# Optimization experiments

Hardware: AMD Instinct MI355X
Metric: run time of the kernel (lower is better)

Reference implementation:

```python
import jax, jax.numpy as jnp
import numpy as np

PROCESSING_STEPS = 3


def setup_inputs() -> dict:
    key = jax.random.key(0)
    ks = jax.random.split(key, 6)
    N, D, G = 500000, 128, 4096
    x = jax.random.normal(ks[0], (N, D), dtype=jnp.float32)
    # torch LSTM param layout: [4*hidden, input] and [4*hidden, hidden], gates i,f,g,o
    s = 1.0 / np.sqrt(D)
    W_ih = jax.random.uniform(ks[1], (4 * D, 2 * D), minval=-s, maxval=s, dtype=jnp.float32)
    W_hh = jax.random.uniform(ks[2], (4 * D, D), minval=-s, maxval=s, dtype=jnp.float32)
    b_ih = jax.random.uniform(ks[3], (4 * D,), minval=-s, maxval=s, dtype=jnp.float32)
    b_hh = jax.random.uniform(ks[4], (4 * D,), minval=-s, maxval=s, dtype=jnp.float32)
    index = jnp.sort(jax.random.randint(ks[5], (N,), 0, G, dtype=jnp.int64))
    return {"x": x, "W_ih": W_ih, "W_hh": W_hh, "b_ih": b_ih, "b_hh": b_hh,
            "index": index, "dim_size": G}


def _lstm_cell(inp, h, c, W_ih, W_hh, b_ih, b_hh):
    gates = inp @ W_ih.T + h @ W_hh.T + (b_ih + b_hh)  # [G, 4D]
    i, f, g, o = jnp.split(gates, 4, axis=-1)
    c = jax.nn.sigmoid(f) * c + jax.nn.sigmoid(i) * jnp.tanh(g)
    h = jax.nn.sigmoid(o) * jnp.tanh(c)
    return h, c


def reference(x, W_ih, W_hh, b_ih, b_hh, index, dim_size):
    N, D = x.shape
    h = jnp.zeros((dim_size, D), dtype=x.dtype)
    c = jnp.zeros((dim_size, D), dtype=x.dtype)
    q_star = jnp.zeros((dim_size, 2 * D), dtype=x.dtype)
    for _ in range(PROCESSING_STEPS):
        h, c = _lstm_cell(q_star, h, c, W_ih, W_hh, b_ih, b_hh)
        q = h  # [G, D]
        e = jnp.sum(x * q[index], axis=-1)  # [N]
        # segment softmax (numerically stable)
        m = jax.ops.segment_max(e, index, num_segments=dim_size)
        m = jnp.where(jnp.isfinite(m), m, 0.0)  # guard empty segments
        ex = jnp.exp(e - m[index])
        s = jax.ops.segment_sum(ex, index, num_segments=dim_size)
        a = ex / jnp.maximum(s, 1e-16)[index]  # [N]
        r = jax.ops.segment_sum(a[:, None] * x, index, num_segments=dim_size)  # [G, D]
        q_star = jnp.concatenate([q, r], axis=-1)
    return q_star
```

## Files before the change

### kernel.cpp

```cpp
#include <hip/hip_runtime.h>
#include <math.h>

#define D 128

__device__ __forceinline__ float sigmoidf_(float x) { return 1.f / (1.f + __expf(-x)); }

__global__ void seg_bounds_kernel(const int* __restrict__ idx, int N, int G,
                                  int* __restrict__ seg_off) {
    int g = blockIdx.x * blockDim.x + threadIdx.x;
    if (g > G) return;
    int lo = 0, hi = N;
    while (lo < hi) {
        int mid = (lo + hi) >> 1;
        if (idx[mid] < g) lo = mid + 1; else hi = mid;
    }
    seg_off[g] = lo;
}

__global__ void prep_wc_kernel(const float* __restrict__ W_ih, const float* __restrict__ W_hh,
                               float* __restrict__ Wc) {
    int t = blockIdx.x * blockDim.x + threadIdx.x;
    if (t >= 4 * D * D) return;
    int j = t >> 7;
    int k = t & (D - 1);
    Wc[t] = W_ih[(size_t)j * (2 * D) + k] + W_hh[t];
}

__global__ void prep_bias_kernel(const float* __restrict__ b_ih, const float* __restrict__ b_hh,
                                 float* __restrict__ b_sum, float* __restrict__ h1,
                                 float* __restrict__ c1) {
    int t = threadIdx.x;
    float b = b_ih[t] + b_hh[t];
    b_sum[t] = b;
    if (t < D) {
        float bi = b_ih[t] + b_hh[t];
        float bg = b_ih[2 * D + t] + b_hh[2 * D + t];
        float bo = b_ih[3 * D + t] + b_hh[3 * D + t];
        float c = sigmoidf_(bi) * tanhf(bg);
        c1[t] = c;
        h1[t] = sigmoidf_(bo) * tanhf(c);
    }
}

__global__ void base2_kernel(const float* __restrict__ Wc, const float* __restrict__ b_sum,
                             const float* __restrict__ h1, float* __restrict__ base2) {
    __shared__ float hs[D];
    int j = blockIdx.x * 256 + threadIdx.x;
    if (threadIdx.x < D) hs[threadIdx.x] = h1[threadIdx.x];
    __syncthreads();
    float acc = 0.f;
    const float4* w4 = (const float4*)(Wc + (size_t)j * D);
#pragma unroll 8
    for (int k4 = 0; k4 < D / 4; ++k4) {
        float4 w = w4[k4];
        const float* hp = &hs[k4 * 4];
        acc += w.x * hp[0] + w.y * hp[1] + w.z * hp[2] + w.w * hp[3];
    }
    base2[j] = b_sum[j] + acc;
}

__global__ __launch_bounds__(64) void attn_kernel(
    const float* __restrict__ x,
    const int* __restrict__ seg_off,
    const float* __restrict__ q,
    int q_stride,
    float* __restrict__ r_out, int r_stride,
    int G) {
    int g = blockIdx.x;
    if (g >= G) return;
    int lane = threadIdx.x;
    const float2* x2 = (const float2*)x;
    const float2* q2 = (const float2*)(q + (size_t)g * q_stride);
    float2 qv = q2[lane];
    int start = seg_off[g], end = seg_off[g + 1];

    float m = -INFINITY, s = 0.f;
    float2 acc; acc.x = 0.f; acc.y = 0.f;

    int n = start;
    for (; n + 2 <= end; n += 2) {
        float2 x0 = x2[(size_t)n * 64 + lane];
        float2 x1 = x2[(size_t)(n + 1) * 64 + lane];
        float p0 = x0.x * qv.x + x0.y * qv.y;
        float p1 = x1.x * qv.x + x1.y * qv.y;
#pragma unroll
        for (int off = 1; off < 64; off <<= 1) {
            p0 += __shfl_xor(p0, off);
            p1 += __shfl_xor(p1, off);
        }
        float mn = fmaxf(m, fmaxf(p0, p1));
        float al = __expf(m - mn);
        float w0 = __expf(p0 - mn);
        float w1 = __expf(p1 - mn);
        s = s * al + w0 + w1;
        acc.x = acc.x * al + w0 * x0.x + w1 * x1.x;
        acc.y = acc.y * al + w0 * x0.y + w1 * x1.y;
        m = mn;
    }
    if (n < end) {
        float2 x0 = x2[(size_t)n * 64 + lane];
        float p0 = x0.x * qv.x + x0.y * qv.y;
#pragma unroll
        for (int off = 1; off < 64; off <<= 1) p0 += __shfl_xor(p0, off);
        float mn = fmaxf(m, p0);
        float al = __expf(m - mn);
        float w0 = __expf(p0 - mn);
        s = s * al + w0;
        acc.x = acc.x * al + w0 * x0.x;
        acc.y = acc.y * al + w0 * x0.y;
    }
    float inv = 1.f / fmaxf(s, 1e-16f);
    float2 r; r.x = acc.x * inv; r.y = acc.y * inv;
    *(float2*)&r_out[(size_t)g * r_stride + 2 * lane] = r;
}

__global__ __launch_bounds__(256) void gates_gemm_kernel(
    const float* __restrict__ A1,
    const float* __restrict__ W1,
    const float* __restrict__ A2,
    const float* __restrict__ W2,
    int sW2,
    const float* __restrict__ bias,
    float* __restrict__ gates) {
    __shared__ float As[16][132];
    __shared__ float Ws[16][132];
    int t = threadIdx.x;
    int tx = t & 15, ty = t >> 4;
    int g0 = blockIdx.x * 128, j0 = blockIdx.y * 128;
    int lr = t >> 1;
    int lk = (t & 1) * 8;

    float acc[8][8];
#pragma unroll
    for (int i = 0; i < 8; ++i)
#pragma unroll
        for (int j = 0; j < 8; ++j) acc[i][j] = 0.f;

    for (int phase = 0; phase < 2; ++phase) {
        const float* A = phase ? A2 : A1;
        if (A == nullptr) continue;
        const float* W = phase ? W2 : W1;
        int sW = phase ? sW2 : D;
        for (int kk = 0; kk < D; kk += 16) {
            float4 a0 = *(const float4*)&A[(size_t)(g0 + lr) * D + kk + lk];
            float4 a1 = *(const float4*)&A[(size_t)(g0 + lr) * D + kk + lk + 4];
            float4 w0 = *(const float4*)&W[(size_t)(j0 + lr) * sW + kk + lk];
            float4 w1 = *(const float4*)&W[(size_t)(j0 + lr) * sW + kk + lk + 4];
            __syncthreads();
            As[lk + 0][lr] = a0.x; As[lk + 1][lr] = a0.y; As[lk + 2][lr] = a0.z; As[lk + 3][lr] = a0.w;
            As[lk + 4][lr] = a1.x; As[lk + 5][lr] = a1.y; As[lk + 6][lr] = a1.z; As[lk + 7][lr] = a1.w;
            Ws[lk + 0][lr] = w0.x; Ws[lk + 1][lr] = w0.y; Ws[lk + 2][lr] = w0.z; Ws[lk + 3][lr] = w0.w;
            Ws[lk + 4][lr] = w1.x; Ws[lk + 5][lr] = w1.y; Ws[lk + 6][lr] = w1.z; Ws[lk + 7][lr] = w1.w;
            __syncthreads();
#pragma unroll
            for (int k = 0; k < 16; ++k) {
                float4 a0v = *(const float4*)&As[k][ty * 8];
                float4 a1v = *(const float4*)&As[k][ty * 8 + 4];
                float4 b0v = *(const float4*)&Ws[k][tx * 8];
                float4 b1v = *(const float4*)&Ws[k][tx * 8 + 4];
                float av[8] = {a0v.x, a0v.y, a0v.z, a0v.w, a1v.x, a1v.y, a1v.z, a1v.w};
                float bv[8] = {b0v.x, b0v.y, b0v.z, b0v.w, b1v.x, b1v.y, b1v.z, b1v.w};
#pragma unroll
                for (int i = 0; i < 8; ++i)
#pragma unroll
                    for (int j = 0; j < 8; ++j)
                        acc[i][j] = fmaf(av[i], bv[j], acc[i][j]);
            }
        }
    }
#pragma unroll
    for (int i = 0; i < 8; ++i) {
        size_t row = (size_t)(g0 + ty * 8 + i);
        float4 o0, o1;
        int jb = j0 + tx * 8;
        o0.x = acc[i][0] + bias[jb + 0]; o0.y = acc[i][1] + bias[jb + 1];
        o0.z = acc[i][2] + bias[jb + 2]; o0.w = acc[i][3] + bias[jb + 3];
        o1.x = acc[i][4] + bias[jb + 4]; o1.y = acc[i][5] + bias[jb + 5];
        o1.z = acc[i][6] + bias[jb + 6]; o1.w = acc[i][7] + bias[jb + 7];
        *(float4*)&gates[row * 512 + jb] = o0;
        *(float4*)&gates[row * 512 + jb + 4] = o1;
    }
}

__global__ void cell_kernel(const float* __restrict__ gates,
                            const float* __restrict__ c_prev, int c_stride,
                            float* __restrict__ c_out,
                            float* __restrict__ h_out, int h_stride,
                            int total) {
    int t = blockIdx.x * blockDim.x + threadIdx.x;
    if (t >= total) return;
    int g = t >> 7, k = t & (D - 1);
    const float* grow = gates + (size_t)g * 512;
    float ig = grow[k];
    float fg = grow[D + k];
    float gg = grow[2 * D + k];
    float og = grow[3 * D + k];
    float cp = c_prev[(size_t)g * c_stride + k];
    float c = sigmoidf_(fg) * cp + sigmoidf_(ig) * tanhf(gg);
    float h = sigmoidf_(og) * tanhf(c);
    c_out[t] = c;
    h_out[(size_t)g * h_stride + k] = h;
}

extern "C" void kernel_launch(void* const* d_in, const int* in_sizes, int n_in,
                              void* d_out, int out_size, void* d_ws, size_t ws_size,
                              hipStream_t stream) {
    const float* x      = (const float*)d_in[0];
    const float* W_ih   = (const float*)d_in[1];
    const float* W_hh   = (const float*)d_in[2];
    const float* b_ih   = (const float*)d_in[3];
    const float* b_hh   = (const float*)d_in[4];
    const int*   index  = (const int*)d_in[5];
    int N = in_sizes[5];
    int G = out_size / (2 * D);
    float* out = (float*)d_out;

    float* ws = (float*)d_ws;
    float* Wc     = ws;
    float* b_sum  = Wc + 4 * D * D;
    float* h1     = b_sum + 4 * D;
    float* c1     = h1 + D;
    float* base2  = c1 + D;
    float* r1     = base2 + 4 * D;
    float* h2     = r1 + (size_t)G * D;
    float* c2     = h2 + (size_t)G * D;
    float* r2     = c2 + (size_t)G * D;
    float* gatesb = r2 + (size_t)G * D;
    int* seg_off  = (int*)(gatesb + (size_t)G * 4 * D);
    float* c3     = r1;

    seg_bounds_kernel<<<(G + 1 + 255) / 256, 256, 0, stream>>>(index, N, G, seg_off);
    prep_wc_kernel<<<(4 * D * D + 255) / 256, 256, 0, stream>>>(W_ih, W_hh, Wc);
    prep_bias_kernel<<<1, 512, 0, stream>>>(b_ih, b_hh, b_sum, h1, c1);
    base2_kernel<<<2, 256, 0, stream>>>(Wc, b_sum, h1, base2);

    attn_kernel<<<G, 64, 0, stream>>>(x, seg_off, h1, 0, r1, D, G);

    gates_gemm_kernel<<<dim3(G / 128, 4), 256, 0, stream>>>(
        nullptr, Wc, r1, W_ih + D, 2 * D, base2, gatesb);
    cell_kernel<<<(G * D + 255) / 256, 256, 0, stream>>>(gatesb, c1, 0, c2, h2, D, G * D);
    attn_kernel<<<G, 64, 0, stream>>>(x, seg_off, h2, D, r2, D, G);

    gates_gemm_kernel<<<dim3(G / 128, 4), 256, 0, stream>>>(
        h2, Wc, r2, W_ih + D, 2 * D, b_sum, gatesb);
    cell_kernel<<<(G * D + 255) / 256, 256, 0, stream>>>(gatesb, c2, D, c3, out, 2 * D, G * D);
    attn_kernel<<<G, 64, 0, stream>>>(x, seg_off, out, 2 * D, out + D, 2 * D, G);
}
```

Measured before the change: 581.2 us.

## Split each segment's attention across four waves with float4 loads and prefetch

The attention kernel now uses 256 threads per segment instead of 64. Each of four wavefronts handles a contiguous quarter of the segment's rows, and the partial online-softmax states (max, sum, accumulator) are merged through shared memory. Within a wave, each half-wave processes one row with float4 loads, and the next pair of rows is prefetched in software. The aim is more memory-level parallelism on the bandwidth-bound x streaming, with a shorter shuffle reduction. In exchange it adds a block-level sync, shared-memory merge overhead, and more threads per small segment (about 122 rows per segment).

```diff
diff --git a/kernel.cpp b/kernel.cpp
--- a/kernel.cpp
+++ b/kernel.cpp
@@ -59,7 +59,7 @@
     base2[j] = b_sum[j] + acc;
 }
 
-__global__ __launch_bounds__(64) void attn_kernel(
+__global__ __launch_bounds__(256) void attn_kernel(
     const float* __restrict__ x,
     const int* __restrict__ seg_off,
     const float* __restrict__ q,
@@ -68,50 +68,82 @@
     int G) {
     int g = blockIdx.x;
     if (g >= G) return;
-    int lane = threadIdx.x;
-    const float2* x2 = (const float2*)x;
-    const float2* q2 = (const float2*)(q + (size_t)g * q_stride);
-    float2 qv = q2[lane];
+    int tid = threadIdx.x;
+    int wave = tid >> 6, lane = tid & 63;
+    int half = lane >> 5;
+    int col4 = lane & 31;
+
+    __shared__ float sm[4], ss[4];
+    __shared__ float sacc[4][D];
+
     int start = seg_off[g], end = seg_off[g + 1];
+    int count = end - start;
+    int chunk = (count + 3) >> 2;
+    int wsr = start + wave * chunk;
+    int wer = min(wsr + chunk, end);
+
+    const float4* x4 = (const float4*)x;
+    const float4* q4 = (const float4*)(q + (size_t)g * q_stride);
+    float4 qv = q4[col4];
 
     float m = -INFINITY, s = 0.f;
-    float2 acc; acc.x = 0.f; acc.y = 0.f;
-
-    int n = start;
-    for (; n + 2 <= end; n += 2) {
-        float2 x0 = x2[(size_t)n * 64 + lane];
-        float2 x1 = x2[(size_t)(n + 1) * 64 + lane];
-        float p0 = x0.x * qv.x + x0.y * qv.y;
-        float p1 = x1.x * qv.x + x1.y * qv.y;
-#pragma unroll
-        for (int off = 1; off < 64; off <<= 1) {
-            p0 += __shfl_xor(p0, off);
-            p1 += __shfl_xor(p1, off);
+    float4 acc = {0.f, 0.f, 0.f, 0.f};
+
+    if (wsr < wer) {
+        int r0 = wsr + half; r0 = r0 < wer ? r0 : wer - 1;
+        float4 xv = x4[(size_t)r0 * 32 + col4];
+        for (int n = wsr; n < wer; n += 2) {
+            int r2 = n + 2 + half; r2 = r2 < wer ? r2 : wer - 1;
+            float4 xn = x4[(size_t)r2 * 32 + col4];
+
+            float p = xv.x * qv.x + xv.y * qv.y + xv.z * qv.z + xv.w * qv.w;
+            p += __shfl_xor(p, 1);
+            p += __shfl_xor(p, 2);
+            p += __shfl_xor(p, 4);
+            p += __shfl_xor(p, 8);
+            p += __shfl_xor(p, 16);
+            float po = __shfl_xor(p, 32);
+            float p0 = half ? po : p;
+            float p1 = half ? p : po;
+            if (n + 1 >= wer) p1 = -INFINITY;
+
+            float mn = fmaxf(m, fmaxf(p0, p1));
+            float al = __expf(m - mn);
+            float w0 = __expf(p0 - mn);
+            float w1 = __expf(p1 - mn);
+            float wsel = half ? w1 : w0;
+            s = s * al + w0 + w1;
+            acc.x = acc.x * al + wsel * xv.x;
+            acc.y = acc.y * al + wsel * xv.y;
+            acc.z = acc.z * al + wsel * xv.z;
+            acc.w = acc.w * al + wsel * xv.w;
+            m = mn;
+            xv = xn;
         }
-        float mn = fmaxf(m, fmaxf(p0, p1));
-        float al = __expf(m - mn);
-        float w0 = __expf(p0 - mn);
-        float w1 = __expf(p1 - mn);
-        s = s * al + w0 + w1;
-        acc.x = acc.x * al + w0 * x0.x + w1 * x1.x;
-        acc.y = acc.y * al + w0 * x0.y + w1 * x1.y;
-        m = mn;
-    }
-    if (n < end) {
-        float2 x0 = x2[(size_t)n * 64 + lane];
-        float p0 = x0.x * qv.x + x0.y * qv.y;
-#pragma unroll
-        for (int off = 1; off < 64; off <<= 1) p0 += __shfl_xor(p0, off);
-        float mn = fmaxf(m, p0);
-        float al = __expf(m - mn);
-        float w0 = __expf(p0 - mn);
-        s = s * al + w0;
-        acc.x = acc.x * al + w0 * x0.x;
-        acc.y = acc.y * al + w0 * x0.y;
-    }
-    float inv = 1.f / fmaxf(s, 1e-16f);
-    float2 r; r.x = acc.x * inv; r.y = acc.y * inv;
-    *(float2*)&r_out[(size_t)g * r_stride + 2 * lane] = r;
+    }
+    acc.x += __shfl_xor(acc.x, 32);
+    acc.y += __shfl_xor(acc.y, 32);
+    acc.z += __shfl_xor(acc.z, 32);
+    acc.w += __shfl_xor(acc.w, 32);
+
+    if (lane == 0) { sm[wave] = m; ss[wave] = s; }
+    if (half == 0) *(float4*)&sacc[wave][col4 * 4] = acc;
+    __syncthreads();
+
+    if (tid < D) {
+        float m0 = sm[0], m1 = sm[1], m2 = sm[2], m3 = sm[3];
+        float mstar = fmaxf(fmaxf(m0, m1), fmaxf(m2, m3));
+        float r = 0.f;
+        if (mstar > -INFINITY) {
+            float e0 = __expf(m0 - mstar), e1 = __expf(m1 - mstar);
+            float e2 = __expf(m2 - mstar), e3 = __expf(m3 - mstar);
+            float stot = ss[0] * e0 + ss[1] * e1 + ss[2] * e2 + ss[3] * e3;
+            float at = sacc[0][tid] * e0 + sacc[1][tid] * e1
+                     + sacc[2][tid] * e2 + sacc[3][tid] * e3;
+            r = at / fmaxf(stot, 1e-16f);
+        }
+        r_out[(size_t)g * r_stride + tid] = r;
+    }
 }
 
 __global__ __launch_bounds__(256) void gates_gemm_kernel(
@@ -234,15 +266,15 @@
     prep_bias_kernel<<<1, 512, 0, stream>>>(b_ih, b_hh, b_sum, h1, c1);
     base2_kernel<<<2, 256, 0, stream>>>(Wc, b_sum, h1, base2);
 
-    attn_kernel<<<G, 64, 0, stream>>>(x, seg_off, h1, 0, r1, D, G);
+    attn_kernel<<<G, 256, 0, stream>>>(x, seg_off, h1, 0, r1, D, G);
 
     gates_gemm_kernel<<<dim3(G / 128, 4), 256, 0, stream>>>(
         nullptr, Wc, r1, W_ih + D, 2 * D, base2, gatesb);
     cell_kernel<<<(G * D + 255) / 256, 256, 0, stream>>>(gatesb, c1, 0, c2, h2, D, G * D);
-    attn_kernel<<<G, 64, 0, stream>>>(x, seg_off, h2, D, r2, D, G);
+    attn_kernel<<<G, 256, 0, stream>>>(x, seg_off, h2, D, r2, D, G);
 
     gates_gemm_kernel<<<dim3(G / 128, 4), 256, 0, stream>>>(
         h2, Wc, r2, W_ih + D, 2 * D, b_sum, gatesb);
     cell_kernel<<<(G * D + 255) / 256, 256, 0, stream>>>(gatesb, c2, D, c3, out, 2 * D, G * D);
-    attn_kernel<<<G, 64, 0, stream>>>(x, seg_off, out, 2 * D, out + D, 2 * D, G);
-}
+    attn_kernel<<<G, 256, 0, stream>>>(x, seg_off, out, 2 * D, out + D, 2 * D, G);
+}
```

Measured after the change: 529.6 us. 8.9% less time.
